# Kernel tuning notes

Hardware: AMD Instinct MI355X
Metric: run time of the kernel (lower is better)

The kernel has to match this reference:

```python
import jax, jax.numpy as jnp
import numpy as np

B, N, C, H = 4, 4096, 1024, 16
D = C // H


def setup_inputs() -> dict:
    key = jax.random.key(0)
    ks = jax.random.split(key, 15)
    s = 0.02
    f = lambda k, shp: jax.random.normal(k, shp, dtype=jnp.float32) * s
    return {
        "x": f(ks[0], (B, N, C)),
        "qkv_w": f(ks[1], (C, 3 * C)),
        "qkv_b": f(ks[2], (3 * C,)),
        "out_w": f(ks[3], (C, C)),
        "out_b": f(ks[4], (C,)),
        # NB: original code dynamically re-creates position_bias as (1, N, H, H)
        # because q/k/v are never transposed to (B,H,N,D); attention runs over heads.
        "pos_bias": f(ks[5], (1, N, H, H)),
        "conv_w": f(ks[6], (C, C)),
        "conv_b": f(ks[7], (C,)),
        "pw_w": f(ks[8], (C, C, 1)),   # Conv1d kernel_size=1: (out, in, k)
        "pw_b": f(ks[9], (C,)),
        "dw_w": f(ks[10], (C, 1, 3)),  # depthwise Conv1d groups=C: (out, in/groups=1, k)
        "dw_b": f(ks[11], (C,)),
        "tok_w": f(ks[12], (C, C)),
        "tok_b": f(ks[13], (C,)),
    }


def reference(x, qkv_w, qkv_b, out_w, out_b, pos_bias,
              conv_w, conv_b, pw_w, pw_b, dw_w, dw_b, tok_w, tok_b):
    b, n, c = x.shape
    h = pos_bias.shape[2]
    d = c // h
    scale = d ** (-0.5)

    # ---- attention branch (faithful to source: heads axis is attended over) ----
    qkv = (x @ qkv_w + qkv_b).reshape(b, n, h, 3 * d)
    q, k, v = jnp.split(qkv, 3, axis=-1)  # each (B, N, H, D)
    scores = jnp.einsum("bnhd,bngd->bnhg", q, k) * scale + pos_bias  # (B, N, H, H)
    attn_w = jax.nn.softmax(scores, axis=-1)
    attn = jnp.einsum("bnhg,bngd->bnhd", attn_w, v).reshape(b, n, c)
    attn = attn @ out_w + out_b

    # ---- convolutional branch ----
    xc = x @ conv_w + conv_b            # (B, N, C)
    xc = xc.transpose(0, 2, 1)          # (B, C, N)
    dn = ("NCH", "OIH", "NCH")
    xc = jax.lax.conv_general_dilated(xc, pw_w, (1,), [(0, 0)],
                                      dimension_numbers=dn) + pw_b[None, :, None]
    xc = jax.lax.conv_general_dilated(xc, dw_w, (1,), [(1, 1)],
                                      dimension_numbers=dn,
                                      feature_group_count=c) + dw_b[None, :, None]
    xc = xc.transpose(0, 2, 1) @ tok_w + tok_b  # (B, N, C)

    return attn + xc
```

## Files before the change

### kernel.cpp

```cpp
#include <hip/hip_runtime.h>
#include <hip/hip_bf16.h>


typedef __attribute__((ext_vector_type(8))) short sh8;
typedef __attribute__((ext_vector_type(4))) float f4;

__device__ __forceinline__ float bf2f(short s) {
  unsigned u = ((unsigned)(unsigned short)s) << 16;
  return __builtin_bit_cast(float, u);
}
__device__ __forceinline__ short f2bf(float f) {
  return __builtin_bit_cast(short, __float2bfloat16(f));
}
__device__ __forceinline__ void g2l16(const void* g, void* l) {
  __builtin_amdgcn_global_load_lds(
      (const __attribute__((address_space(1))) unsigned int*)g,
      (__attribute__((address_space(3))) unsigned int*)l, 16, 0, 0);
}

__global__ __launch_bounds__(256) void cvt3(
    const float* __restrict__ x, const float* __restrict__ conv_w,
    const float* __restrict__ pw_w, short* __restrict__ xb,
    short* __restrict__ convb, short* __restrict__ pwb) {
  int i = blockIdx.x * 256 + threadIdx.x;
  const float* src;
  short* dst;
  int off;
  if (i < 2097152) {
    src = x; dst = xb; off = i;
  } else if (i < 2228224) {
    src = conv_w; dst = convb; off = i - 2097152;
  } else {
    src = pw_w; dst = pwb; off = i - 2228224;
  }
  float4 a = ((const float4*)src)[off * 2];
  float4 b = ((const float4*)src)[off * 2 + 1];
  sh8 o;
  o[0] = f2bf(a.x); o[1] = f2bf(a.y); o[2] = f2bf(a.z); o[3] = f2bf(a.w);
  o[4] = f2bf(b.x); o[5] = f2bf(b.y); o[6] = f2bf(b.z); o[7] = f2bf(b.w);
  ((sh8*)dst)[off] = o;
}

__global__ __launch_bounds__(256) void transpose_f32_bf16(
    const float* __restrict__ src, short* __restrict__ dst,
    int N, int ldd, int coff) {
  __shared__ float tile[32][33];
  int kb = blockIdx.y * 32, nb = blockIdx.x * 32;
  int tx = threadIdx.x, ty = threadIdx.y;
#pragma unroll
  for (int j = 0; j < 32; j += 8)
    tile[ty + j][tx] = src[(size_t)(kb + ty + j) * N + nb + tx];
  __syncthreads();
#pragma unroll
  for (int j = 0; j < 32; j += 8)
    dst[(size_t)(nb + ty + j) * ldd + coff + kb + tx] = f2bf(tile[tx][ty + j]);
}

__global__ __launch_bounds__(256) void transpose2(
    const float* __restrict__ out_w, const float* __restrict__ tok_w,
    short* __restrict__ dst) {
  __shared__ float tile[32][33];
  const float* src = blockIdx.z ? tok_w : out_w;
  int coff = blockIdx.z ? 1024 : 0;
  int kb = blockIdx.y * 32, nb = blockIdx.x * 32;
  int tx = threadIdx.x, ty = threadIdx.y;
#pragma unroll
  for (int j = 0; j < 32; j += 8)
    tile[ty + j][tx] = src[(size_t)(kb + ty + j) * 1024 + nb + tx];
  __syncthreads();
#pragma unroll
  for (int j = 0; j < 32; j += 8)
    dst[(size_t)(nb + ty + j) * 2048 + coff + kb + tx] = f2bf(tile[tx][ty + j]);
}

__global__ __launch_bounds__(256) void prep_misc(
    const float* __restrict__ pw_w, const float* __restrict__ conv_b,
    const float* __restrict__ pw_b, const float* __restrict__ qkv_b,
    const float* __restrict__ out_b, const float* __restrict__ tok_b,
    const float* __restrict__ dw_w, const float* __restrict__ dw_b,
    float* __restrict__ bias4, float* __restrict__ bcat,
    float* __restrict__ dw0, float* __restrict__ dw1,
    float* __restrict__ dw2, float* __restrict__ dwb) {
  int o = blockIdx.x;
  if (o < 1024) {
    float part = 0.f;
    for (int i = threadIdx.x; i < 1024; i += 256)
      part += pw_w[(size_t)o * 1024 + i] * conv_b[i];
#pragma unroll
    for (int off = 32; off >= 1; off >>= 1) part += __shfl_down(part, off);
    __shared__ float red[4];
    int wid = threadIdx.x >> 6, lane = threadIdx.x & 63;
    if (lane == 0) red[wid] = part;
    __syncthreads();
    if (threadIdx.x == 0) {
      float s = red[0] + red[1] + red[2] + red[3];
      bias4[3072 + o] = s + pw_b[o];
      bcat[o] = out_b[o] + tok_b[o];
      dw0[o] = dw_w[o * 3 + 0];
      dw1[o] = dw_w[o * 3 + 1];
      dw2[o] = dw_w[o * 3 + 2];
      dwb[o] = dw_b[o];
    }
  }
  if (threadIdx.x == 0) bias4[o] = qkv_b[o];
}

template <int OUT_BF16>
__global__ __launch_bounds__(256, 2) void gemm128(
    const short* __restrict__ A, const short* __restrict__ Bt,
    void* __restrict__ Cp, const float* __restrict__ bias, int K, int ldc) {
  __shared__ short As[128 * 32];
  __shared__ short Bs[128 * 32];
  const int wid = threadIdx.x >> 6, lane = threadIdx.x & 63;
  const int bm = blockIdx.y, bn = blockIdx.x;
  const int wr = wid >> 1, wc = wid & 1;
  const size_t abase = (size_t)bm * 128 * K;
  const size_t bbase = (size_t)bn * 128 * K;
  const int r16 = lane & 15, ko = (lane >> 4) * 8;

  f4 acc[4][4] = {};

  for (int k0 = 0; k0 < K; k0 += 32) {
    __syncthreads();
#pragma unroll
    for (int c = 0; c < 2; ++c) {
      int ch = c * 256 + wid * 64 + lane;
      int row = ch >> 2, kc = (ch & 3) * 8;
      g2l16(A + abase + (size_t)row * K + k0 + kc, &As[ch * 8]);
      g2l16(Bt + bbase + (size_t)row * K + k0 + kc, &Bs[ch * 8]);
    }
    __syncthreads();
    sh8 af[4], bf[4];
#pragma unroll
    for (int i = 0; i < 4; ++i)
      af[i] = *(const sh8*)&As[(wr * 64 + i * 16 + r16) * 32 + ko];
#pragma unroll
    for (int j = 0; j < 4; ++j)
      bf[j] = *(const sh8*)&Bs[(wc * 64 + j * 16 + r16) * 32 + ko];
#pragma unroll
    for (int i = 0; i < 4; ++i)
#pragma unroll
      for (int j = 0; j < 4; ++j)
        acc[i][j] = __builtin_amdgcn_mfma_f32_16x16x32_bf16(af[i], bf[j],
                                                            acc[i][j], 0, 0, 0);
  }

  const int crow = wr * 64 + (lane >> 4) * 4;
  const int ccol = wc * 64 + r16;
#pragma unroll
  for (int i = 0; i < 4; ++i) {
#pragma unroll
    for (int j = 0; j < 4; ++j) {
      int col = bn * 128 + ccol + j * 16;
      float bv = bias ? bias[col] : 0.f;
#pragma unroll
      for (int r = 0; r < 4; ++r) {
        int row = bm * 128 + crow + i * 16 + r;
        float v = acc[i][j][r] + bv;
        if (OUT_BF16)
          ((short*)Cp)[(size_t)row * ldc + col] = f2bf(v);
        else
          ((float*)Cp)[(size_t)row * ldc + col] = v;
      }
    }
  }
}

template <int OUT_BF16>
__global__ __launch_bounds__(512, 2) void gemm8p(
    const short* __restrict__ A, const short* __restrict__ Bt,
    void* __restrict__ Cp, const float* __restrict__ bias,
    int K, int ldc, int nbn) {
  __shared__ short lds[65536];
  const int tid = threadIdx.x;
  const int lane = tid & 63, wid = tid >> 6;
  const int wr = wid >> 2, wc = wid & 3;
  const int r16 = lane & 15;
  const int kidx = ((lane >> 4) ^ ((r16 >> 1) & 3)) << 3;

  const int cpx = gridDim.x >> 3;
  const int swz = (blockIdx.x & 7) * cpx + (blockIdx.x >> 3);
  const int bm = swz / nbn, bn = swz % nbn;

  const short* Ag = A + (size_t)bm * 256 * K;
  const short* Bg = Bt + (size_t)bn * 256 * K;

  int goff0, goff1, loff0, loff1;
  {
    int s0 = tid, row0 = s0 >> 2;
    int kc0 = (s0 & 3) ^ ((row0 >> 1) & 3);
    goff0 = row0 * K + kc0 * 8;
    loff0 = s0 * 8;
    int s1 = 512 + tid, row1 = s1 >> 2;
    int kc1 = (s1 & 3) ^ ((row1 >> 1) & 3);
    goff1 = row1 * K + kc1 * 8;
    loff1 = s1 * 8;
  }

  f4 acc[8][4] = {};
  const int NT = K >> 6;

#define SOP(GB, DS)                                         \
  do {                                                      \
    g2l16((GB) + goff0, (DS) + loff0);                      \
    g2l16((GB) + goff1, (DS) + loff1);                      \
  } while (0)

#define PHASE_SYNC()                                        \
  do {                                                      \
    __builtin_amdgcn_sched_barrier(0);                      \
    __builtin_amdgcn_s_barrier();                           \
    __builtin_amdgcn_sched_barrier(0);                      \
  } while (0)

  {
    short* b0 = &lds[0];
    short* b1 = &lds[32768];
    SOP(Ag, b0 + 0);
    SOP(Bg, b0 + 16384);
    SOP(Ag + 32, b0 + 8192);
    SOP(Bg + 32, b0 + 24576);
    SOP(Bg + 64, b1 + 16384);
    SOP(Ag + 64, b1 + 0);
  }
  asm volatile("s_waitcnt vmcnt(4)" ::: "memory");
  PHASE_SYNC();

  for (int t = 0; t < NT; ++t) {
    const int b = t & 1;
    const short* buf = &lds[b * 32768];
    short* bufC = &lds[b * 32768];
    short* bufN = &lds[(b ^ 1) * 32768];
    const int t1 = (t + 1 < NT) ? t + 1 : 0;
    const int t2 = (t + 2 < NT) ? t + 2 : 0;

    sh8 af[8], bfr[4];

#pragma unroll
    for (int i = 0; i < 4; ++i)
      af[i] = *(const sh8*)&buf[(wr * 128 + i * 16 + r16) * 32 + kidx];
#pragma unroll
    for (int j = 0; j < 4; ++j)
      bfr[j] = *(const sh8*)&buf[16384 + (wc * 64 + j * 16 + r16) * 32 + kidx];
    SOP(Ag + t1 * 64 + 32, bufN + 8192);
    SOP(Bg + t1 * 64 + 32, bufN + 24576);
    PHASE_SYNC();
    __builtin_amdgcn_s_setprio(1);
#pragma unroll
    for (int i = 0; i < 4; ++i)
#pragma unroll
      for (int j = 0; j < 4; ++j)
        acc[i][j] = __builtin_amdgcn_mfma_f32_16x16x32_bf16(af[i], bfr[j],
                                                            acc[i][j], 0, 0, 0);
    __builtin_amdgcn_s_setprio(0);
    PHASE_SYNC();

#pragma unroll
    for (int i = 4; i < 8; ++i)
      af[i] = *(const sh8*)&buf[(wr * 128 + i * 16 + r16) * 32 + kidx];
    SOP(Bg + t2 * 64, bufC + 16384);
    PHASE_SYNC();
    __builtin_amdgcn_s_setprio(1);
#pragma unroll
    for (int i = 4; i < 8; ++i)
#pragma unroll
      for (int j = 0; j < 4; ++j)
        acc[i][j] = __builtin_amdgcn_mfma_f32_16x16x32_bf16(af[i], bfr[j],
                                                            acc[i][j], 0, 0, 0);
    __builtin_amdgcn_s_setprio(0);
    PHASE_SYNC();

#pragma unroll
    for (int i = 0; i < 4; ++i)
      af[i] = *(const sh8*)&buf[8192 + (wr * 128 + i * 16 + r16) * 32 + kidx];
#pragma unroll
    for (int j = 0; j < 4; ++j)
      bfr[j] = *(const sh8*)&buf[24576 + (wc * 64 + j * 16 + r16) * 32 + kidx];
    SOP(Ag + t2 * 64, bufC + 0);
    PHASE_SYNC();
    __builtin_amdgcn_s_setprio(1);
#pragma unroll
    for (int i = 0; i < 4; ++i)
#pragma unroll
      for (int j = 0; j < 4; ++j)
        acc[i][j] = __builtin_amdgcn_mfma_f32_16x16x32_bf16(af[i], bfr[j],
                                                            acc[i][j], 0, 0, 0);
    __builtin_amdgcn_s_setprio(0);
    PHASE_SYNC();

#pragma unroll
    for (int i = 4; i < 8; ++i)
      af[i] = *(const sh8*)&buf[8192 + (wr * 128 + i * 16 + r16) * 32 + kidx];
    asm volatile("s_waitcnt vmcnt(4)" ::: "memory");
    PHASE_SYNC();
    __builtin_amdgcn_s_setprio(1);
#pragma unroll
    for (int i = 4; i < 8; ++i)
#pragma unroll
      for (int j = 0; j < 4; ++j)
        acc[i][j] = __builtin_amdgcn_mfma_f32_16x16x32_bf16(af[i], bfr[j],
                                                            acc[i][j], 0, 0, 0);
    __builtin_amdgcn_s_setprio(0);
    PHASE_SYNC();
  }
#undef SOP
#undef PHASE_SYNC

  const int crow0 = bm * 256 + wr * 128 + (lane >> 4) * 4;
  const int ccol0 = bn * 256 + wc * 64 + r16;
  float bv[4];
#pragma unroll
  for (int j = 0; j < 4; ++j) bv[j] = bias ? bias[ccol0 + j * 16] : 0.f;
#pragma unroll
  for (int i = 0; i < 8; ++i) {
#pragma unroll
    for (int r = 0; r < 4; ++r) {
      size_t rowoff = (size_t)(crow0 + i * 16 + r) * ldc + ccol0;
#pragma unroll
      for (int j = 0; j < 4; ++j) {
        float v = acc[i][j][r] + bv[j];
        if (OUT_BF16)
          ((short*)Cp)[rowoff + j * 16] = f2bf(v);
        else
          ((float*)Cp)[rowoff + j * 16] = v;
      }
    }
  }
}

__global__ __launch_bounds__(256) void epilogue(
    const short* __restrict__ qkvx, const float* __restrict__ pos_bias,
    const float* __restrict__ dw0, const float* __restrict__ dw1,
    const float* __restrict__ dw2, const float* __restrict__ dwb,
    short* __restrict__ xcat) {
  __shared__ short sq[4 * 3072];
  __shared__ short slice[6 * 1024];
  int t0 = blockIdx.x * 4;
#pragma unroll
  for (int c = 0; c < 6; ++c) {
    int g = c * 256 + threadIdx.x;
    int tok = (g * 683) >> 18;
    int off = g - tok * 384;
    ((sh8*)sq)[tok * 384 + off] =
        *(const sh8*)(qkvx + (size_t)(t0 + tok) * 4096 + off * 8);
  }
#pragma unroll
  for (int s = 0; s < 3; ++s) {
    int g = s * 256 + threadIdx.x;
    int r = g >> 7, off = g & 127;
    int gr = t0 - 1 + r;
    sh8 v = {};
    if (gr >= 0 && gr < 16384)
      v = *(const sh8*)(qkvx + (size_t)gr * 4096 + 3072 + off * 8);
    ((sh8*)slice)[g] = v;
  }
  __syncthreads();

  int wid = threadIdx.x >> 6, lane = threadIdx.x & 63;
  int t = t0 + wid, n = t & 4095;
  int h = lane >> 2, sub = lane & 3;
  const short* base = sq + wid * 3072 + h * 192;

  float qf[64];
#pragma unroll
  for (int c = 0; c < 8; ++c) {
    sh8 v8 = *(const sh8*)(base + c * 8);
#pragma unroll
    for (int j = 0; j < 8; ++j) qf[c * 8 + j] = bf2f(v8[j]);
  }

  const float* pb = pos_bias + (size_t)n * 256 + h * 16 + sub * 4;
  float p[4];
  float m = -1e30f;
#pragma unroll
  for (int g4 = 0; g4 < 4; ++g4) {
    int g = sub * 4 + g4;
    const short* kk = sq + wid * 3072 + g * 192 + 64;
    float acc = 0.f;
#pragma unroll
    for (int c = 0; c < 8; ++c) {
      sh8 k8 = *(const sh8*)(kk + c * 8);
#pragma unroll
      for (int j = 0; j < 8; ++j) acc += qf[c * 8 + j] * bf2f(k8[j]);
    }
    p[g4] = acc * 0.125f + pb[g4];
    m = fmaxf(m, p[g4]);
  }
  m = fmaxf(m, __shfl_xor(m, 1));
  m = fmaxf(m, __shfl_xor(m, 2));
  float sum = 0.f;
#pragma unroll
  for (int g4 = 0; g4 < 4; ++g4) {
    p[g4] = __expf(p[g4] - m);
    sum += p[g4];
  }
  sum += __shfl_xor(sum, 1);
  sum += __shfl_xor(sum, 2);
  float inv = 1.0f / sum;
#pragma unroll
  for (int g4 = 0; g4 < 4; ++g4) p[g4] *= inv;

  float pall[16];
#pragma unroll
  for (int g = 0; g < 16; ++g)
    pall[g] = __shfl(p[g & 3], (lane & 60) | (g >> 2));

  float o[16] = {};
#pragma unroll
  for (int g = 0; g < 16; ++g) {
    const short* vv = sq + wid * 3072 + g * 192 + 128 + sub * 16;
    sh8 va = *(const sh8*)vv;
    sh8 vb = *(const sh8*)(vv + 8);
#pragma unroll
    for (int j = 0; j < 8; ++j) {
      o[j] += pall[g] * bf2f(va[j]);
      o[8 + j] += pall[g] * bf2f(vb[j]);
    }
  }
  sh8 oa, ob;
#pragma unroll
  for (int j = 0; j < 8; ++j) {
    oa[j] = f2bf(o[j]);
    ob[j] = f2bf(o[8 + j]);
  }
  short* dst = xcat + (size_t)t * 2048 + h * 64 + sub * 16;
  *(sh8*)dst = oa;
  *(sh8*)(dst + 8) = ob;

#pragma unroll
  for (int it = 0; it < 2; ++it) {
    int w = it * 256 + threadIdx.x;
    int tok = w >> 7, co = (w & 127) * 8;
    int tt = t0 + tok, nn = tt & 4095;
    const short* lo8 = slice + tok * 1024 + co;
    const short* mi8 = lo8 + 1024;
    const short* hi8 = lo8 + 2048;
    sh8 lo = (nn > 0) ? *(const sh8*)lo8 : sh8{};
    sh8 mi = *(const sh8*)mi8;
    sh8 hi = (nn < 4095) ? *(const sh8*)hi8 : sh8{};
    sh8 out;
#pragma unroll
    for (int j = 0; j < 8; ++j) {
      float v = dw0[co + j] * bf2f(lo[j]) + dw1[co + j] * bf2f(mi[j]) +
                dw2[co + j] * bf2f(hi[j]) + dwb[co + j];
      out[j] = f2bf(v);
    }
    *(sh8*)(xcat + (size_t)tt * 2048 + 1024 + co) = out;
  }
}

extern "C" void kernel_launch(void* const* d_in, const int* in_sizes, int n_in,
                              void* d_out, int out_size, void* d_ws,
                              size_t ws_size, hipStream_t stream) {
  const float* x      = (const float*)d_in[0];
  const float* qkv_w  = (const float*)d_in[1];
  const float* qkv_b  = (const float*)d_in[2];
  const float* out_w  = (const float*)d_in[3];
  const float* out_b  = (const float*)d_in[4];
  const float* pos_b  = (const float*)d_in[5];
  const float* conv_w = (const float*)d_in[6];
  const float* conv_b = (const float*)d_in[7];
  const float* pw_w   = (const float*)d_in[8];
  const float* pw_b   = (const float*)d_in[9];
  const float* dw_w   = (const float*)d_in[10];
  const float* dw_b   = (const float*)d_in[11];
  const float* tok_w  = (const float*)d_in[12];
  const float* tok_b  = (const float*)d_in[13];

  const int M = 16384;
  char* ws = (char*)d_ws;
  size_t off = 0;
  auto alloc = [&](size_t bytes) -> void* {
    void* p = ws + off;
    off += (bytes + 255) & ~(size_t)255;
    return p;
  };
  short* xb    = (short*)alloc((size_t)M * 1024 * 2);
  short* wbig  = (short*)alloc((size_t)4096 * 1024 * 2);
  short* wcatT = (short*)alloc((size_t)1024 * 2048 * 2);
  short* convb = (short*)alloc((size_t)1024 * 1024 * 2);
  short* pwb   = (short*)alloc((size_t)1024 * 1024 * 2);
  short* qkvx  = (short*)alloc((size_t)M * 4096 * 2);
  short* xcat  = (short*)alloc((size_t)M * 2048 * 2);
  float* bias4 = (float*)alloc(4096 * 4);
  float* bcat  = (float*)alloc(1024 * 4);
  float* dw0   = (float*)alloc(1024 * 4);
  float* dw1   = (float*)alloc(1024 * 4);
  float* dw2   = (float*)alloc(1024 * 4);
  float* dwb   = (float*)alloc(1024 * 4);
  (void)ws_size; (void)in_sizes; (void)n_in; (void)out_size;

  cvt3<<<9216, 256, 0, stream>>>(x, conv_w, pw_w, xb, convb, pwb);
  transpose_f32_bf16<<<dim3(96, 32), dim3(32, 8), 0, stream>>>(qkv_w, wbig, 3072, 1024, 0);
  transpose2<<<dim3(32, 32, 2), dim3(32, 8), 0, stream>>>(out_w, tok_w, wcatT);
  prep_misc<<<3072, 256, 0, stream>>>(pw_w, conv_b, pw_b, qkv_b, out_b, tok_b,
                                      dw_w, dw_b, bias4, bcat, dw0, dw1, dw2, dwb);
  gemm128<1><<<dim3(8, 8), 256, 0, stream>>>(pwb, convb, wbig + (size_t)3072 * 1024,
                                             nullptr, 1024, 1024);

  gemm8p<1><<<1024, 512, 0, stream>>>(xb, wbig, qkvx, bias4, 1024, 4096, 16);

  epilogue<<<4096, 256, 0, stream>>>(qkvx, pos_b, dw0, dw1, dw2, dwb, xcat);

  gemm8p<0><<<256, 512, 0, stream>>>(xcat, wcatT, d_out, bcat, 2048, 1024, 4);
}
```

Measured before the change: 326.4 us.

## Load B fragments directly from global and triple-buffer A in LDS

```diff
diff --git a/kernel.cpp b/kernel.cpp
--- a/kernel.cpp
+++ b/kernel.cpp
@@ -167,11 +167,11 @@
 }
 
 template <int OUT_BF16>
-__global__ __launch_bounds__(512, 2) void gemm8p(
+__global__ __launch_bounds__(512, 2) void gemmBG(
     const short* __restrict__ A, const short* __restrict__ Bt,
     void* __restrict__ Cp, const float* __restrict__ bias,
     int K, int ldc, int nbn) {
-  __shared__ short lds[65536];
+  __shared__ short lds[24576];
   const int tid = threadIdx.x;
   const int lane = tid & 63, wid = tid >> 6;
   const int wr = wid >> 2, wc = wid & 3;
@@ -183,128 +183,98 @@
   const int bm = swz / nbn, bn = swz % nbn;
 
   const short* Ag = A + (size_t)bm * 256 * K;
-  const short* Bg = Bt + (size_t)bn * 256 * K;
-
-  int goff0, goff1, loff0, loff1;
+  const short* Bbase =
+      Bt + (size_t)(bn * 256 + wc * 64 + r16) * K + (lane >> 4) * 8;
+
+  int gA0, lA0, gA1, lA1;
   {
-    int s0 = tid, row0 = s0 >> 2;
-    int kc0 = (s0 & 3) ^ ((row0 >> 1) & 3);
-    goff0 = row0 * K + kc0 * 8;
-    loff0 = s0 * 8;
-    int s1 = 512 + tid, row1 = s1 >> 2;
-    int kc1 = (s1 & 3) ^ ((row1 >> 1) & 3);
-    goff1 = row1 * K + kc1 * 8;
-    loff1 = s1 * 8;
+    int c0 = tid, r0 = c0 >> 2, k0 = (c0 & 3) ^ ((r0 >> 1) & 3);
+    gA0 = r0 * K + k0 * 8;
+    lA0 = c0 * 8;
+    int c1 = 512 + tid, r1 = c1 >> 2, k1 = (c1 & 3) ^ ((r1 >> 1) & 3);
+    gA1 = r1 * K + k1 * 8;
+    lA1 = c1 * 8;
   }
 
   f4 acc[8][4] = {};
-  const int NT = K >> 6;
-
-#define SOP(GB, DS)                                         \
+  const int NT = K >> 5;
+
+#define STAGE_A(KT, BUF)                                    \
   do {                                                      \
-    g2l16((GB) + goff0, (DS) + loff0);                      \
-    g2l16((GB) + goff1, (DS) + loff1);                      \
+    short* lb = &lds[(BUF) * 8192];                         \
+    const short* ga = Ag + (KT) * 32;                       \
+    g2l16(ga + gA0, lb + lA0);                              \
+    g2l16(ga + gA1, lb + lA1);                              \
   } while (0)
 
-#define PHASE_SYNC()                                        \
+#define LOADB(BF, KT)                                                     \
+  do {                                                                    \
+    _Pragma("unroll")                                                     \
+    for (int j = 0; j < 4; ++j)                                           \
+      BF[j] = *(const sh8*)(Bbase + (size_t)j * 16 * K + (KT) * 32);      \
+  } while (0)
+
+#define LOADA(BUF)                                                        \
+  do {                                                                    \
+    const short* buf_ = &lds[(BUF) * 8192];                               \
+    _Pragma("unroll")                                                     \
+    for (int i = 0; i < 8; ++i)                                           \
+      af[i] = *(const sh8*)&buf_[(wr * 128 + i * 16 + r16) * 32 + kidx];  \
+  } while (0)
+
+#define MFMA32(BF)                                                        \
+  do {                                                                    \
+    __builtin_amdgcn_s_setprio(1);                                        \
+    _Pragma("unroll")                                                     \
+    for (int i = 0; i < 8; ++i)                                           \
+      _Pragma("unroll")                                                   \
+      for (int j = 0; j < 4; ++j)                                         \
+        acc[i][j] = __builtin_amdgcn_mfma_f32_16x16x32_bf16(              \
+            af[i], BF[j], acc[i][j], 0, 0, 0);                            \
+    __builtin_amdgcn_s_setprio(0);                                        \
+  } while (0)
+
+#define BARRIER_FENCED()                                    \
   do {                                                      \
     __builtin_amdgcn_sched_barrier(0);                      \
     __builtin_amdgcn_s_barrier();                           \
     __builtin_amdgcn_sched_barrier(0);                      \
   } while (0)
 
-  {
-    short* b0 = &lds[0];
-    short* b1 = &lds[32768];
-    SOP(Ag, b0 + 0);
-    SOP(Bg, b0 + 16384);
-    SOP(Ag + 32, b0 + 8192);
-    SOP(Bg + 32, b0 + 24576);
-    SOP(Bg + 64, b1 + 16384);
-    SOP(Ag + 64, b1 + 0);
-  }
-  asm volatile("s_waitcnt vmcnt(4)" ::: "memory");
-  PHASE_SYNC();
-
-  for (int t = 0; t < NT; ++t) {
-    const int b = t & 1;
-    const short* buf = &lds[b * 32768];
-    short* bufC = &lds[b * 32768];
-    short* bufN = &lds[(b ^ 1) * 32768];
-    const int t1 = (t + 1 < NT) ? t + 1 : 0;
-    const int t2 = (t + 2 < NT) ? t + 2 : 0;
-
-    sh8 af[8], bfr[4];
-
-#pragma unroll
-    for (int i = 0; i < 4; ++i)
-      af[i] = *(const sh8*)&buf[(wr * 128 + i * 16 + r16) * 32 + kidx];
-#pragma unroll
-    for (int j = 0; j < 4; ++j)
-      bfr[j] = *(const sh8*)&buf[16384 + (wc * 64 + j * 16 + r16) * 32 + kidx];
-    SOP(Ag + t1 * 64 + 32, bufN + 8192);
-    SOP(Bg + t1 * 64 + 32, bufN + 24576);
-    PHASE_SYNC();
-    __builtin_amdgcn_s_setprio(1);
-#pragma unroll
-    for (int i = 0; i < 4; ++i)
-#pragma unroll
-      for (int j = 0; j < 4; ++j)
-        acc[i][j] = __builtin_amdgcn_mfma_f32_16x16x32_bf16(af[i], bfr[j],
-                                                            acc[i][j], 0, 0, 0);
-    __builtin_amdgcn_s_setprio(0);
-    PHASE_SYNC();
-
-#pragma unroll
-    for (int i = 4; i < 8; ++i)
-      af[i] = *(const sh8*)&buf[(wr * 128 + i * 16 + r16) * 32 + kidx];
-    SOP(Bg + t2 * 64, bufC + 16384);
-    PHASE_SYNC();
-    __builtin_amdgcn_s_setprio(1);
-#pragma unroll
-    for (int i = 4; i < 8; ++i)
-#pragma unroll
-      for (int j = 0; j < 4; ++j)
-        acc[i][j] = __builtin_amdgcn_mfma_f32_16x16x32_bf16(af[i], bfr[j],
-                                                            acc[i][j], 0, 0, 0);
-    __builtin_amdgcn_s_setprio(0);
-    PHASE_SYNC();
-
-#pragma unroll
-    for (int i = 0; i < 4; ++i)
-      af[i] = *(const sh8*)&buf[8192 + (wr * 128 + i * 16 + r16) * 32 + kidx];
-#pragma unroll
-    for (int j = 0; j < 4; ++j)
-      bfr[j] = *(const sh8*)&buf[24576 + (wc * 64 + j * 16 + r16) * 32 + kidx];
-    SOP(Ag + t2 * 64, bufC + 0);
-    PHASE_SYNC();
-    __builtin_amdgcn_s_setprio(1);
-#pragma unroll
-    for (int i = 0; i < 4; ++i)
-#pragma unroll
-      for (int j = 0; j < 4; ++j)
-        acc[i][j] = __builtin_amdgcn_mfma_f32_16x16x32_bf16(af[i], bfr[j],
-                                                            acc[i][j], 0, 0, 0);
-    __builtin_amdgcn_s_setprio(0);
-    PHASE_SYNC();
-
-#pragma unroll
-    for (int i = 4; i < 8; ++i)
-      af[i] = *(const sh8*)&buf[8192 + (wr * 128 + i * 16 + r16) * 32 + kidx];
-    asm volatile("s_waitcnt vmcnt(4)" ::: "memory");
-    PHASE_SYNC();
-    __builtin_amdgcn_s_setprio(1);
-#pragma unroll
-    for (int i = 4; i < 8; ++i)
-#pragma unroll
-      for (int j = 0; j < 4; ++j)
-        acc[i][j] = __builtin_amdgcn_mfma_f32_16x16x32_bf16(af[i], bfr[j],
-                                                            acc[i][j], 0, 0, 0);
-    __builtin_amdgcn_s_setprio(0);
-    PHASE_SYNC();
-  }
-#undef SOP
-#undef PHASE_SYNC
+  sh8 af[8], bfrA[4], bfrB[4];
+
+  STAGE_A(0, 0);
+  STAGE_A(1, 1);
+  __builtin_amdgcn_sched_barrier(0);
+  asm volatile("s_waitcnt vmcnt(2)" ::: "memory");
+  BARRIER_FENCED();
+  LOADB(bfrA, 0);
+
+  for (int t = 0; t < NT; t += 2) {
+    {
+      const int kt2 = (t + 2 < NT) ? t + 2 : 0;
+      STAGE_A(kt2, (t + 2) % 3);
+      const int kt1 = (t + 1 < NT) ? t + 1 : 0;
+      LOADB(bfrB, kt1);
+      LOADA(t % 3);
+      MFMA32(bfrA);
+      BARRIER_FENCED();
+    }
+    {
+      const int kt3 = (t + 3 < NT) ? t + 3 : 0;
+      STAGE_A(kt3, (t + 3) % 3);
+      const int kt2 = (t + 2 < NT) ? t + 2 : 0;
+      LOADB(bfrA, kt2);
+      LOADA((t + 1) % 3);
+      MFMA32(bfrB);
+      BARRIER_FENCED();
+    }
+  }
+#undef STAGE_A
+#undef LOADB
+#undef LOADA
+#undef MFMA32
+#undef BARRIER_FENCED
 
   const int crow0 = bm * 256 + wr * 128 + (lane >> 4) * 4;
   const int ccol0 = bn * 256 + wc * 64 + r16;
@@ -498,9 +468,9 @@
   gemm128<1><<<dim3(8, 8), 256, 0, stream>>>(pwb, convb, wbig + (size_t)3072 * 1024,
                                              nullptr, 1024, 1024);
 
-  gemm8p<1><<<1024, 512, 0, stream>>>(xb, wbig, qkvx, bias4, 1024, 4096, 16);
+  gemmBG<1><<<1024, 512, 0, stream>>>(xb, wbig, qkvx, bias4, 1024, 4096, 16);
 
   epilogue<<<4096, 256, 0, stream>>>(qkvx, pos_b, dw0, dw1, dw2, dwb, xcat);
 
-  gemm8p<0><<<256, 512, 0, stream>>>(xcat, wcatT, d_out, bcat, 2048, 1024, 4);
-}
+  gemmBG<0><<<256, 512, 0, stream>>>(xcat, wcatT, d_out, bcat, 2048, 1024, 4);
+}
```

New measurement: 404.7 us. 1.24x slower.
